# Kernel optimization log

Hardware: AMD Instinct MI355X
Metric: run time of the kernel (lower is better)

## Reference

```python
import jax, jax.numpy as jnp
import numpy as np

B, T, D = 64, 64, 256      # batch, decode steps, input_dim == wv_dim
TA = 128                   # encoder (attention) length
U = 256                    # units == att_dim
V = 50257                  # vocab_size


def hard_sigmoid(x):
    # keras hard_sigmoid
    return jnp.clip(0.2 * x + 0.5, 0.0, 1.0)


def setup_inputs() -> dict:
    key = jax.random.key(0)
    ks = jax.random.split(key, 8)
    n = lambda k, shape, sc: (jax.random.normal(k, shape, jnp.float32) * sc)
    return {
        "x": jax.random.normal(ks[0], (B, T, D), jnp.float32),
        "att": jax.random.normal(ks[1], (B, TA, U), jnp.float32),
        "kernel": n(ks[2], (D, 3 * U), 0.05),
        "recurrent_kernel": n(ks[3], (U, 3 * U), 0.05),
        "bias": jnp.zeros((3 * U,), jnp.float32),
        "after_att_kernel": n(ks[4], (U, 2 * U), 0.05),
        "after_att_bias": jnp.zeros((2 * U,), jnp.float32),
        "W_o1": n(ks[5], (U, V), 0.02),
        "embedding": n(ks[6], (V, D), 0.05),  # id2v table (non-trainable)
    }


def reference(x, att, kernel, recurrent_kernel, bias, after_att_kernel,
              after_att_bias, W_o1, embedding):
    u = recurrent_kernel.shape[0]
    # preprocess_input: time-distributed dense for all three gates at once
    xp = jnp.einsum('btd,dk->btk', x, kernel) + bias          # (B,T,3U)
    Kz, Kr, Kh = kernel[:, :u], kernel[:, u:2 * u], kernel[:, 2 * u:]
    Uz, Ur, Uh = (recurrent_kernel[:, :u], recurrent_kernel[:, u:2 * u],
                  recurrent_kernel[:, 2 * u:])
    Wa0, Wa1 = after_att_kernel[:, :u], after_att_kernel[:, u:2 * u]
    ba0, ba1 = after_att_bias[:u], after_att_bias[u:2 * u]

    h0 = jnp.zeros((x.shape[0], u), x.dtype)

    def step(h, xt):
        # attention over encoder outputs using previous hidden state
        e = jax.nn.softmax(jnp.einsum('btd,bd->bt', att, h))   # (B,TA)
        c = jnp.einsum('bt,btd->bd', e, att)                   # (B,U)
        # after-attention dense stack -> vocab distribution
        s = jnp.tanh(c @ Wa0 + ba0)
        s = jnp.tanh(s @ Wa1 + ba1)
        p = jax.nn.softmax(s @ W_o1)                           # (B,V)
        # embedding feedback (soft; hard_argmax=False)
        fb = p @ embedding                                     # (B,D)
        # GRU gates with feedback routed through the input kernel
        xz, xr, xh = xt[:, :u], xt[:, u:2 * u], xt[:, 2 * u:]
        z = hard_sigmoid(xz + fb @ Kz + h @ Uz)
        r = hard_sigmoid(xr + fb @ Kr + h @ Ur)
        hh = jnp.tanh(xh + fb @ Kh + (r * h) @ Uh)
        hn = z * h + (1.0 - z) * hh
        return hn, hn

    _, ys = jax.lax.scan(step, h0, jnp.swapaxes(xp, 0, 1))     # (T,B,U)
    return jnp.swapaxes(ys, 0, 1)                              # (B,T,U)
```

## Files before the change

### kernel.cpp

```cpp
#include <hip/hip_runtime.h>

#define BB 64
#define TT 64
#define DD 256
#define TAA 128
#define UU 256
#define VV 50257
#define NBLK 256
#define NV 208
#define NVK 224
#define W1ROWS 53248
#define EMBCOLS 53248
#define NT 512
#define OFF_W1   0
#define OFF_EMB  54912
#define OFF_P    114304
#define OFF_SA   129152
#define OFF_HL   146048
#define OFF_ZP   147072
#define SMEM_BYTES 147712

typedef __attribute__((ext_vector_type(4))) float floatx4;
typedef unsigned long long ull_t;

__device__ __forceinline__ float bf2f(unsigned short u) {
  union { unsigned int i; float f; } c; c.i = ((unsigned int)u) << 16; return c.f;
}
__device__ __forceinline__ float pklo(unsigned int u) { return __uint_as_float(u << 16); }
__device__ __forceinline__ float pkhi(unsigned int u) { return __uint_as_float(u & 0xffff0000u); }
__device__ __forceinline__ unsigned short f2bf(float f) {
  union { float f; unsigned int i; } c; c.f = f;
  return (unsigned short)((c.i + 0x7fffu + ((c.i >> 16) & 1u)) >> 16);
}
__device__ __forceinline__ float hsig(float x) {
  return fminf(1.0f, fmaxf(0.0f, 0.2f * x + 0.5f));
}
__device__ __forceinline__ unsigned int pk4_fp8(float a, float b, float c, float d) {
  unsigned int r = 0;
  r = __builtin_amdgcn_cvt_pk_fp8_f32(a, b, r, false);
  r = __builtin_amdgcn_cvt_pk_fp8_f32(c, d, r, true);
  return r;
}

__device__ __forceinline__ void st_f(float* p, float v) {
  __hip_atomic_store(p, v, __ATOMIC_RELAXED, __HIP_MEMORY_SCOPE_AGENT);
}
__device__ __forceinline__ float ld_f(const float* p) {
  return __hip_atomic_load(p, __ATOMIC_RELAXED, __HIP_MEMORY_SCOPE_AGENT);
}
__device__ __forceinline__ void st_u16(unsigned short* p, unsigned short v) {
  __hip_atomic_store(p, v, __ATOMIC_RELAXED, __HIP_MEMORY_SCOPE_AGENT);
}
__device__ __forceinline__ void st_u32(unsigned int* p, unsigned int v) {
  __hip_atomic_store(p, v, __ATOMIC_RELAXED, __HIP_MEMORY_SCOPE_AGENT);
}
__device__ __forceinline__ unsigned int ld_u32(const unsigned int* p) {
  return __hip_atomic_load(p, __ATOMIC_RELAXED, __HIP_MEMORY_SCOPE_AGENT);
}
__device__ __forceinline__ ull_t ld_u64(const ull_t* p) {
  return __hip_atomic_load(p, __ATOMIC_RELAXED, __HIP_MEMORY_SCOPE_AGENT);
}

__device__ __forceinline__ void gbar(ull_t* bar, int phase) {
  asm volatile("s_waitcnt vmcnt(0)" ::: "memory");
  __syncthreads();
  if (threadIdx.x == 0) {
    ull_t* myc = (ull_t*)((char*)bar + 128 * (1 + (blockIdx.x & 7)));
    ull_t t1 = __hip_atomic_fetch_add(myc, 1ull, __ATOMIC_RELAXED,
                                      __HIP_MEMORY_SCOPE_AGENT) + 1ull;
    if (t1 == (ull_t)(32 * phase)) {
      __hip_atomic_fetch_add(bar, 1ull, __ATOMIC_RELAXED, __HIP_MEMORY_SCOPE_AGENT);
    }
    while (__hip_atomic_load(bar, __ATOMIC_RELAXED, __HIP_MEMORY_SCOPE_AGENT) <
           (ull_t)(8 * phase))
      __builtin_amdgcn_s_sleep(4);
  }
  __syncthreads();
}


__global__ void k_f2bf(const float* __restrict__ in, unsigned short* __restrict__ out, int n) {
  int i = blockIdx.x * 256 + threadIdx.x;
  int stride = gridDim.x * 256;
  for (; i < n; i += stride) out[i] = f2bf(in[i]);
}

__global__ void k_pack(const float* __restrict__ kern, const float* __restrict__ rk,
                       unsigned int* __restrict__ kzr, unsigned int* __restrict__ uzr,
                       unsigned int* __restrict__ khu) {
  const int k = blockIdx.x;
  const int out = threadIdx.x;
  const float* kr0 = kern + (size_t)k * 768;
  const float* rr0 = rk + (size_t)k * 768;
  kzr[k * 256 + out] = (unsigned)f2bf(kr0[out]) | ((unsigned)f2bf(kr0[256 + out]) << 16);
  uzr[k * 256 + out] = (unsigned)f2bf(rr0[out]) | ((unsigned)f2bf(rr0[256 + out]) << 16);
  khu[k * 256 + out] = (unsigned)f2bf(kr0[512 + out]) | ((unsigned)f2bf(rr0[512 + out]) << 16);
}

__global__ void k_tw1(const float* __restrict__ w, unsigned int* __restrict__ o) {
  __shared__ float tile[32][33];
  const int bx = blockIdx.x, by = blockIdx.y;
  const int tx = threadIdx.x, ty = threadIdx.y;
#pragma unroll
  for (int i = 0; i < 4; ++i) {
    int k = by * 32 + ty + i * 8;
    int v = bx * 32 + tx;
    tile[ty + i * 8][tx] = (v < VV) ? w[(size_t)k * VV + v] : 0.0f;
  }
  __syncthreads();
  const int t = ty * 32 + tx;
  const int vl = t >> 3;
  const int cg = t & 7;
  unsigned int pk = pk4_fp8(tile[cg * 4 + 0][vl], tile[cg * 4 + 1][vl],
                            tile[cg * 4 + 2][vl], tile[cg * 4 + 3][vl]);
  o[(size_t)(bx * 32 + vl) * 64 + by * 8 + cg] = pk;
}

__global__ void k_temb(const float* __restrict__ e, unsigned int* __restrict__ o) {
  __shared__ float tile[32][33];
  const int bx = blockIdx.x, by = blockIdx.y;
  const int tx = threadIdx.x, ty = threadIdx.y;
#pragma unroll
  for (int i = 0; i < 4; ++i) {
    int v = bx * 32 + ty + i * 8;
    int d = by * 32 + tx;
    tile[ty + i * 8][tx] = (v < VV) ? e[(size_t)v * 256 + d] : 0.0f;
  }
  __syncthreads();
  const int t = ty * 32 + tx;
  const int dl = t >> 3;
  const int vg = t & 7;
  unsigned int pk = pk4_fp8(tile[vg * 4 + 0][dl], tile[vg * 4 + 1][dl],
                            tile[vg * 4 + 2][dl], tile[vg * 4 + 3][dl]);
  o[(size_t)(by * 32 + dl) * 13312 + bx * 8 + vg] = pk;
}

__global__ void k_xp(const float* __restrict__ x, const float* __restrict__ kern,
                     const float* __restrict__ bias, float* __restrict__ xp) {
  __shared__ float xs[256][20];
  const int r0 = blockIdx.x * 16;
  const int tid = threadIdx.x;
  for (int idx = tid; idx < 16 * 256; idx += 256) {
    int rr = idx >> 8;
    int k = idx & 255;
    xs[k][rr] = x[(size_t)(r0 + rr) * 256 + k];
  }
  __syncthreads();
  float acc[16][3];
#pragma unroll
  for (int rr = 0; rr < 16; ++rr) {
    acc[rr][0] = bias[tid];
    acc[rr][1] = bias[256 + tid];
    acc[rr][2] = bias[512 + tid];
  }
  for (int k = 0; k < 256; ++k) {
    float k0 = kern[k * 768 + tid];
    float k1 = kern[k * 768 + 256 + tid];
    float k2 = kern[k * 768 + 512 + tid];
#pragma unroll
    for (int rr = 0; rr < 16; ++rr) {
      float xv = xs[k][rr];
      acc[rr][0] = fmaf(xv, k0, acc[rr][0]);
      acc[rr][1] = fmaf(xv, k1, acc[rr][1]);
      acc[rr][2] = fmaf(xv, k2, acc[rr][2]);
    }
  }
  for (int rr = 0; rr < 16; ++rr) {
    xp[(size_t)(r0 + rr) * 768 + tid] = acc[rr][0];
    xp[(size_t)(r0 + rr) * 768 + 256 + tid] = acc[rr][1];
    xp[(size_t)(r0 + rr) * 768 + 512 + tid] = acc[rr][2];
  }
}


__global__ void __launch_bounds__(NT, 2) gru_main(
    const float* __restrict__ att,
    const float* __restrict__ aab,
    const unsigned int* __restrict__ kzr,
    const unsigned int* __restrict__ uzr,
    const unsigned int* __restrict__ khu,
    const unsigned short* __restrict__ aabf,
    const float* __restrict__ xp,
    const unsigned int* __restrict__ w1g,
    const unsigned int* __restrict__ embg,
    unsigned int* __restrict__ s8,
    unsigned short* __restrict__ pfb,
    float* __restrict__ psum,
    float* __restrict__ fbp4,
    ull_t* __restrict__ hflag,
    ull_t* __restrict__ bar,
    float* __restrict__ y)
{
  extern __shared__ char smem[];
  char* w1p  = smem + OFF_W1;
  char* embp = smem + OFF_EMB;
  char* Pp   = smem + OFF_P;
  char* sAp  = smem + OFF_SA;
  float* red4  = (float*)(smem + OFF_SA);
  float* fbL   = (float*)(smem + OFF_SA + 8192);
  float* rhL   = (float*)(smem + OFF_SA + 9216);
  float* cL    = (float*)(smem + OFF_SA + 10240);
  float* s1L   = (float*)(smem + OFF_SA + 11264);
  float* s2L   = (float*)(smem + OFF_SA + 12288);
  float* eL    = (float*)(smem + OFF_SA + 13312);
  float* zredL = (float*)(smem + OFF_SA + 13824);
  float* hL    = (float*)(smem + OFF_HL);
  float* zpartL= (float*)(smem + OFF_ZP);

  const int blk = blockIdx.x;
  const int tid = threadIdx.x;
  const int b = blk;
  const int vbase = blk * NV;

  const int w = tid >> 6;
  const int lane = tid & 63;
  const int w2 = w & 3;
  const int half = w >> 2;
  const int lq = lane >> 4;
  const int li = lane & 15;
  const int hb = blk & 63;
  const int hq = blk >> 6;

  {
    unsigned int* dst = (unsigned int*)w1p;
    for (int i = tid; i < NV * 64; i += NT) {
      int r = i >> 6, c = i & 63;
      dst[r * 66 + c] = w1g[(size_t)(vbase + r) * 64 + c];
    }
    unsigned int* ed = (unsigned int*)embp;
    for (int i = tid; i < 256 * 52; i += NT) {
      int r = i / 52, c = i - r * 52;
      ed[r * 58 + c] = embg[(size_t)r * 13312 + blk * 52 + c];
    }
    for (int i = tid; i < 256 * 6; i += NT) {
      int r = i / 6, c = i - r * 6;
      ed[r * 58 + 52 + c] = 0u;
    }
    unsigned int* Pd = (unsigned int*)Pp;
    for (int i = tid; i < 64 * 6; i += NT) {
      int r = i / 6, c = i - r * 6;
      Pd[r * 58 + 52 + c] = 0u;
    }
  }

  auto attention = [&]() {
    {
      const int r = tid >> 2, q = tid & 3;
      const float* ar = att + (size_t)(b * TAA + r) * DD + q * 64;
      const float* hp = hL + q * 64;
      float l0 = 0.f, l1 = 0.f;
#pragma unroll
      for (int dd = 0; dd < 64; dd += 8) {
        float4 a0 = *reinterpret_cast<const float4*>(ar + dd);
        float4 a1 = *reinterpret_cast<const float4*>(ar + dd + 4);
        l0 += a0.x * hp[dd] + a0.y * hp[dd + 1] + a0.z * hp[dd + 2] + a0.w * hp[dd + 3];
        l1 += a1.x * hp[dd + 4] + a1.y * hp[dd + 5] + a1.z * hp[dd + 6] + a1.w * hp[dd + 7];
      }
      float s = l0 + l1;
      s += __shfl_xor(s, 1);
      s += __shfl_xor(s, 2);
      if (q == 0) eL[r] = s;
    }
    __syncthreads();
    if (tid < 64) {
      float l0 = eL[tid], l1 = eL[tid + 64];
      float m = fmaxf(l0, l1);
#pragma unroll
      for (int off = 32; off > 0; off >>= 1) m = fmaxf(m, __shfl_xor(m, off));
      float e0 = __expf(l0 - m), e1 = __expf(l1 - m);
      float s = e0 + e1;
#pragma unroll
      for (int off = 32; off > 0; off >>= 1) s += __shfl_xor(s, off);
      float inv = 1.0f / s;
      eL[tid] = e0 * inv;
      eL[tid + 64] = e1 * inv;
    }
    __syncthreads();
    {
      const int d = tid & 255, g = tid >> 8;
      const float* ab = att + (size_t)b * TAA * DD + d;
      float c0 = 0.f, c1 = 0.f;
#pragma unroll 4
      for (int ta = g * 64; ta < g * 64 + 64; ta += 2) {
        c0 += eL[ta] * ab[(size_t)ta * DD];
        c1 += eL[ta + 1] * ab[(size_t)(ta + 1) * DD];
      }
      red4[tid] = c0 + c1;
    }
    __syncthreads();
    if (tid < 256) cL[tid] = red4[tid] + red4[tid + 256];
    __syncthreads();
    {
      const int out = tid & 255, g = tid >> 8;
      float a0 = g ? 0.f : aab[out], a1 = 0.f;
      for (int k = g * 128; k < g * 128 + 128; k += 2) {
        a0 += cL[k] * bf2f(aabf[k * 512 + out]);
        a1 += cL[k + 1] * bf2f(aabf[(k + 1) * 512 + out]);
      }
      red4[tid] = a0 + a1;
    }
    __syncthreads();
    if (tid < 256) s1L[tid] = tanhf(red4[tid] + red4[tid + 256]);
    __syncthreads();
    {
      const int out = tid & 255, g = tid >> 8;
      float a0 = g ? 0.f : aab[256 + out], a1 = 0.f;
      for (int k = g * 128; k < g * 128 + 128; k += 2) {
        a0 += s1L[k] * bf2f(aabf[k * 512 + 256 + out]);
        a1 += s1L[k + 1] * bf2f(aabf[(k + 1) * 512 + 256 + out]);
      }
      red4[tid] = a0 + a1;
    }
    __syncthreads();
    if (tid < 256) s2L[tid] = tanhf(red4[tid] + red4[tid + 256]);
    __syncthreads();
    if (tid < 64) {
      unsigned int pk = pk4_fp8(s2L[4 * tid], s2L[4 * tid + 1],
                                s2L[4 * tid + 2], s2L[4 * tid + 3]);
      st_u32(s8 + b * 64 + tid, pk);
    }
  };

  auto helper_reduce = [&]() {
    {
      const int gl = tid >> 6;
      const int dq = tid & 63;
      float a0 = 0, a1 = 0, a2 = 0, a3 = 0;
      const ull_t* base = (const ull_t*)pfb + (size_t)hb * (256 * 64) + dq;
      const int g0 = hq * 64 + gl;
#pragma unroll
      for (int i = 0; i < 8; ++i) {
        ull_t u = ld_u64(base + (size_t)(g0 + i * 8) * 64);
        a0 += __uint_as_float((unsigned)(u << 16));
        a1 += __uint_as_float((unsigned)u & 0xffff0000u);
        a2 += __uint_as_float(((unsigned)(u >> 16)) & 0xffff0000u);
        a3 += __uint_as_float(((unsigned)(u >> 32)) & 0xffff0000u);
      }
      *reinterpret_cast<float4*>(red4 + gl * 256 + dq * 4) =
          make_float4(a0, a1, a2, a3);
    }
    __syncthreads();
    if (tid < 256) {
      float s = 0.f;
#pragma unroll
      for (int j = 0; j < 8; ++j) s += red4[tid + j * 256];
      st_f(fbp4 + ((size_t)hb * 4 + hq) * 256 + tid, s);
    }
    asm volatile("s_waitcnt vmcnt(0)" ::: "memory");
    __syncthreads();
    if (tid == 0)
      __hip_atomic_fetch_add(hflag + (size_t)hb * 16, 1ull, __ATOMIC_RELAXED,
                             __HIP_MEMORY_SCOPE_AGENT);
  };

  auto ca_step = [&](int t) {
    if (tid < 256) zredL[tid] = ld_f(psum + b * 256 + tid);
    __syncthreads();
    if (tid < 64) {
      float z2 = zredL[tid] + zredL[tid + 64] + zredL[tid + 128] + zredL[tid + 192];
#pragma unroll
      for (int off = 32; off > 0; off >>= 1) z2 += __shfl_xor(z2, off);
      if (tid == 0) zredL[0] = z2;
    }
    if (tid == 0) {
      while (__hip_atomic_load(hflag + (size_t)b * 16, __ATOMIC_RELAXED,
                               __HIP_MEMORY_SCOPE_AGENT) < (ull_t)(4 * (t + 1)))
        __builtin_amdgcn_s_sleep(2);
    }
    __syncthreads();
    if (tid < 256) {
      float invZ = 1.0f / zredL[0];
      const float* fp = fbp4 + (size_t)b * 1024;
      fbL[tid] = (ld_f(fp + tid) + ld_f(fp + 256 + tid) +
                  ld_f(fp + 512 + tid) + ld_f(fp + 768 + tid)) * invZ;
    }
    __syncthreads();
    const float* xprow = xp + (size_t)(b * 64 + t) * 768;
    const int out = tid & 255, g = tid >> 8;
    float z0 = g ? 0.f : xprow[out], z1 = 0.f;
    float r0 = g ? 0.f : xprow[256 + out], r1 = 0.f;
    for (int k = g * 128; k < g * 128 + 128; k += 2) {
      float fb0 = fbL[k], h0 = hL[k], fb1 = fbL[k + 1], h1 = hL[k + 1];
      unsigned a0 = kzr[k * 256 + out];
      unsigned b0 = uzr[k * 256 + out];
      unsigned a1 = kzr[(k + 1) * 256 + out];
      unsigned b1 = uzr[(k + 1) * 256 + out];
      z0 += fb0 * pklo(a0) + h0 * pklo(b0);
      r0 += fb0 * pkhi(a0) + h0 * pkhi(b0);
      z1 += fb1 * pklo(a1) + h1 * pklo(b1);
      r1 += fb1 * pkhi(a1) + h1 * pkhi(b1);
    }
    red4[tid] = z0 + z1;
    red4[512 + tid] = r0 + r1;
    __syncthreads();
    float zf = 0.f;
    if (tid < 256) {
      zf = red4[tid] + red4[tid + 256];
      float rf = red4[512 + tid] + red4[768 + tid];
      rhL[tid] = hsig(rf) * hL[tid];
    }
    __syncthreads();
    {
      float hp0 = g ? 0.f : xprow[512 + out], hp1 = 0.f;
      for (int k = g * 128; k < g * 128 + 128; k += 2) {
        unsigned c0 = khu[k * 256 + out];
        unsigned c1 = khu[(k + 1) * 256 + out];
        hp0 += fbL[k] * pklo(c0) + rhL[k] * pkhi(c0);
        hp1 += fbL[k + 1] * pklo(c1) + rhL[k + 1] * pkhi(c1);
      }
      red4[1024 + tid] = hp0 + hp1;
    }
    __syncthreads();
    if (tid < 256) {
      float hh = tanhf(red4[1024 + tid] + red4[1280 + tid]);
      float z = hsig(zf);
      float hn = z * hL[tid] + (1.0f - z) * hh;
      y[(size_t)(b * 64 + t) * 256 + tid] = hn;
      hL[tid] = hn;
    }
    __syncthreads();
  };

  auto b_phase = [&]() {
    {
      unsigned int* sd = (unsigned int*)sAp;
      for (int i = tid; i < 4096; i += NT) {
        int r = i >> 6, c = i & 63;
        sd[r * 66 + c] = ld_u32(s8 + i);
      }
    }
    __syncthreads();
    long afr[8];
#pragma unroll
    for (int kk = 0; kk < 8; ++kk)
      afr[kk] = *reinterpret_cast<const long*>(sAp + (16 * w2 + li) * 264 + kk * 32 + lq * 8);
    float sacc[4] = {0.f, 0.f, 0.f, 0.f};
    const int vt0 = half ? 7 : 0;
    const int vt1 = half ? 13 : 7;
    for (int vt = vt0; vt < vt1; ++vt) {
      floatx4 lacc = (floatx4){0.f, 0.f, 0.f, 0.f};
#pragma unroll
      for (int kk = 0; kk < 8; ++kk) {
        long bfr = *reinterpret_cast<const long*>(w1p + (vt * 16 + li) * 264 + kk * 32 + lq * 8);
        lacc = __builtin_amdgcn_mfma_f32_16x16x32_fp8_fp8(afr[kk], bfr, lacc, 0, 0, 0);
      }
      const int v = vbase + vt * 16 + li;
      const bool ok = (v < VV);
#pragma unroll
      for (int q = 0; q < 4; ++q) {
        float p = ok ? __expf(lacc[q]) : 0.0f;
        sacc[q] += p;
        unsigned int pb = __builtin_amdgcn_cvt_pk_fp8_f32(p, 0.f, 0u, false);
        Pp[(16 * w2 + lq * 4 + q) * 232 + vt * 16 + li] = (char)(pb & 0xff);
      }
    }
#pragma unroll
    for (int q = 0; q < 4; ++q) {
      float s = sacc[q];
      s += __shfl_xor(s, 1);
      s += __shfl_xor(s, 2);
      s += __shfl_xor(s, 4);
      s += __shfl_xor(s, 8);
      if (li == 0) zpartL[(16 * w2 + lq * 4 + q) * 2 + half] = s;
    }
    __syncthreads();
    if (tid < 64) st_f(psum + tid * 256 + blk, zpartL[2 * tid] + zpartL[2 * tid + 1]);
    long pfr[7];
#pragma unroll
    for (int kk = 0; kk < 7; ++kk)
      pfr[kk] = *reinterpret_cast<const long*>(Pp + (16 * w2 + li) * 232 + kk * 32 + lq * 8);
    const int dt0 = half * 8;
#pragma unroll 4
    for (int dt = dt0; dt < dt0 + 8; ++dt) {
      floatx4 f = (floatx4){0.f, 0.f, 0.f, 0.f};
#pragma unroll
      for (int kk = 0; kk < 7; ++kk) {
        long efr = *reinterpret_cast<const long*>(embp + (dt * 16 + li) * 232 + kk * 32 + lq * 8);
        f = __builtin_amdgcn_mfma_f32_16x16x32_fp8_fp8(pfr[kk], efr, f, 0, 0, 0);
      }
#pragma unroll
      for (int q = 0; q < 4; ++q) {
        int row = 16 * w2 + lq * 4 + q;
        st_u16(pfb + ((size_t)(row * 256 + blk)) * 256 + dt * 16 + li, f2bf(f[q]));
      }
    }
  };

  __syncthreads();
  if (blk < BB) {
    if (tid < 256) hL[tid] = 0.0f;
    __syncthreads();
    attention();
  }
  gbar(bar, 1);
  for (int t = 0; t < TT; ++t) {
    b_phase();
    gbar(bar, 2 + 2 * t);
    helper_reduce();
    if (blk < BB) {
      ca_step(t);
      if (t + 1 < TT) attention();
    }
    gbar(bar, 3 + 2 * t);
  }
}


extern "C" void kernel_launch(void* const* d_in, const int* in_sizes, int n_in,
                              void* d_out, int out_size, void* d_ws, size_t ws_size,
                              hipStream_t stream) {
  const float* x    = (const float*)d_in[0];
  const float* att  = (const float*)d_in[1];
  const float* kern = (const float*)d_in[2];
  const float* rk   = (const float*)d_in[3];
  const float* bias = (const float*)d_in[4];
  const float* aak  = (const float*)d_in[5];
  const float* aab  = (const float*)d_in[6];
  const float* w1   = (const float*)d_in[7];
  const float* emb  = (const float*)d_in[8];
  float* y = (float*)d_out;

  char* ws = (char*)d_ws;
  size_t o = 0;
  auto alloc = [&](size_t bytes) {
    char* p = ws + o;
    o += (bytes + 255) & ~(size_t)255;
    return p;
  };
  ull_t* bar   = (ull_t*)alloc(2048);
  ull_t* hflag = (ull_t*)alloc(8192);
  unsigned int* w1g  = (unsigned int*)alloc((size_t)W1ROWS * 256);
  unsigned int* embg = (unsigned int*)alloc((size_t)256 * EMBCOLS);
  unsigned int* kzr  = (unsigned int*)alloc((size_t)256 * 256 * 4);
  unsigned int* uzr  = (unsigned int*)alloc((size_t)256 * 256 * 4);
  unsigned int* khu  = (unsigned int*)alloc((size_t)256 * 256 * 4);
  unsigned short* aabf = (unsigned short*)alloc((size_t)131072 * 2);
  float* xp  = (float*)alloc((size_t)4096 * 768 * 4);
  unsigned int* s8 = (unsigned int*)alloc((size_t)64 * 64 * 4);
  unsigned short* pfb = (unsigned short*)alloc((size_t)64 * 256 * 256 * 2);
  float* psum = (float*)alloc((size_t)64 * 256 * 4);
  float* fbp4 = (float*)alloc((size_t)64 * 4 * 256 * 4);
  (void)ws_size; (void)in_sizes; (void)n_in; (void)out_size;

  static bool attr_done = false;
  if (!attr_done) {
    hipFuncSetAttribute((const void*)gru_main,
                        hipFuncAttributeMaxDynamicSharedMemorySize, SMEM_BYTES);
    attr_done = true;
  }

  hipMemsetAsync(bar, 0, 2048 + 8192, stream);
  hipLaunchKernelGGL(k_pack, dim3(256), dim3(256), 0, stream, kern, rk, kzr, uzr, khu);
  hipLaunchKernelGGL(k_f2bf, dim3(512), dim3(256), 0, stream, aak, aabf, 131072);
  hipLaunchKernelGGL(k_tw1, dim3(1664, 8), dim3(32, 8), 0, stream, w1, w1g);
  hipLaunchKernelGGL(k_temb, dim3(1664, 8), dim3(32, 8), 0, stream, emb, embg);
  hipLaunchKernelGGL(k_xp, dim3(256), dim3(256), 0, stream, x, kern, bias, xp);
  hipLaunchKernelGGL(gru_main, dim3(NBLK), dim3(NT), SMEM_BYTES, stream,
                     att, aab, kzr, uzr, khu, aabf, xp, w1g, embg, s8, pfb, psum,
                     fbp4, hflag, bar, y);
}
```

Before: 2.882 ms.

## Let owner blocks reduce their own feedback quarter, pack dense weights in pairs

Owner blocks (blk < 64) now reduce the first quarter of their own feedback partials locally into shared memory instead of waiting on a helper block to write it to global memory. The flag wait therefore drops from four helper arrivals to three. The after-attention weights are packed as bf16 pairs so each load serves two k rows. The b_phase also reads the s8 A-fragments straight from global memory instead of staging them through shared memory behind an extra barrier. The trade-off is more work on the critical-path owner blocks and uncoalesced 64-bit global loads for the fragments.

```diff
diff --git a/kernel.cpp b/kernel.cpp
--- a/kernel.cpp
+++ b/kernel.cpp
@@ -79,12 +79,6 @@
 }
 
 
-__global__ void k_f2bf(const float* __restrict__ in, unsigned short* __restrict__ out, int n) {
-  int i = blockIdx.x * 256 + threadIdx.x;
-  int stride = gridDim.x * 256;
-  for (; i < n; i += stride) out[i] = f2bf(in[i]);
-}
-
 __global__ void k_pack(const float* __restrict__ kern, const float* __restrict__ rk,
                        unsigned int* __restrict__ kzr, unsigned int* __restrict__ uzr,
                        unsigned int* __restrict__ khu) {
@@ -97,6 +91,13 @@
   khu[k * 256 + out] = (unsigned)f2bf(kr0[512 + out]) | ((unsigned)f2bf(rr0[512 + out]) << 16);
 }
 
+__global__ void k_aap(const float* __restrict__ aak, unsigned int* __restrict__ aap2) {
+  const int idx = blockIdx.x * 256 + threadIdx.x;
+  const int k2 = idx >> 9, col = idx & 511;
+  aap2[idx] = (unsigned)f2bf(aak[(size_t)(2 * k2) * 512 + col]) |
+              ((unsigned)f2bf(aak[(size_t)(2 * k2 + 1) * 512 + col]) << 16);
+}
+
 __global__ void k_tw1(const float* __restrict__ w, unsigned int* __restrict__ o) {
   __shared__ float tile[32][33];
   const int bx = blockIdx.x, by = blockIdx.y;
@@ -179,7 +180,7 @@
     const unsigned int* __restrict__ kzr,
     const unsigned int* __restrict__ uzr,
     const unsigned int* __restrict__ khu,
-    const unsigned short* __restrict__ aabf,
+    const unsigned int* __restrict__ aap2,
     const float* __restrict__ xp,
     const unsigned int* __restrict__ w1g,
     const unsigned int* __restrict__ embg,
@@ -195,7 +196,6 @@
   char* w1p  = smem + OFF_W1;
   char* embp = smem + OFF_EMB;
   char* Pp   = smem + OFF_P;
-  char* sAp  = smem + OFF_SA;
   float* red4  = (float*)(smem + OFF_SA);
   float* fbL   = (float*)(smem + OFF_SA + 8192);
   float* rhL   = (float*)(smem + OFF_SA + 9216);
@@ -204,6 +204,7 @@
   float* s2L   = (float*)(smem + OFF_SA + 12288);
   float* eL    = (float*)(smem + OFF_SA + 13312);
   float* zredL = (float*)(smem + OFF_SA + 13824);
+  float* ownq  = (float*)(smem + OFF_SA + 14848);
   float* hL    = (float*)(smem + OFF_HL);
   float* zpartL= (float*)(smem + OFF_ZP);
 
@@ -293,9 +294,10 @@
     {
       const int out = tid & 255, g = tid >> 8;
       float a0 = g ? 0.f : aab[out], a1 = 0.f;
-      for (int k = g * 128; k < g * 128 + 128; k += 2) {
-        a0 += cL[k] * bf2f(aabf[k * 512 + out]);
-        a1 += cL[k + 1] * bf2f(aabf[(k + 1) * 512 + out]);
+      for (int k2 = g * 64; k2 < g * 64 + 64; ++k2) {
+        unsigned u = aap2[k2 * 512 + out];
+        a0 += cL[2 * k2] * pklo(u);
+        a1 += cL[2 * k2 + 1] * pkhi(u);
       }
       red4[tid] = a0 + a1;
     }
@@ -305,9 +307,10 @@
     {
       const int out = tid & 255, g = tid >> 8;
       float a0 = g ? 0.f : aab[256 + out], a1 = 0.f;
-      for (int k = g * 128; k < g * 128 + 128; k += 2) {
-        a0 += s1L[k] * bf2f(aabf[k * 512 + 256 + out]);
-        a1 += s1L[k + 1] * bf2f(aabf[(k + 1) * 512 + 256 + out]);
+      for (int k2 = g * 64; k2 < g * 64 + 64; ++k2) {
+        unsigned u = aap2[k2 * 512 + 256 + out];
+        a0 += s1L[2 * k2] * pklo(u);
+        a1 += s1L[2 * k2 + 1] * pkhi(u);
       }
       red4[tid] = a0 + a1;
     }
@@ -321,24 +324,26 @@
     }
   };
 
+  auto quarter_partials = [&](int thb, int thq) {
+    const int gl = tid >> 6;
+    const int dq = tid & 63;
+    float a0 = 0, a1 = 0, a2 = 0, a3 = 0;
+    const ull_t* base = (const ull_t*)pfb + (size_t)thb * (256 * 64) + dq;
+    const int g0 = thq * 64 + gl;
+#pragma unroll
+    for (int i = 0; i < 8; ++i) {
+      ull_t u = ld_u64(base + (size_t)(g0 + i * 8) * 64);
+      a0 += __uint_as_float((unsigned)(u << 16));
+      a1 += __uint_as_float((unsigned)u & 0xffff0000u);
+      a2 += __uint_as_float(((unsigned)(u >> 16)) & 0xffff0000u);
+      a3 += __uint_as_float(((unsigned)(u >> 32)) & 0xffff0000u);
+    }
+    *reinterpret_cast<float4*>(red4 + gl * 256 + dq * 4) =
+        make_float4(a0, a1, a2, a3);
+  };
+
   auto helper_reduce = [&]() {
-    {
-      const int gl = tid >> 6;
-      const int dq = tid & 63;
-      float a0 = 0, a1 = 0, a2 = 0, a3 = 0;
-      const ull_t* base = (const ull_t*)pfb + (size_t)hb * (256 * 64) + dq;
-      const int g0 = hq * 64 + gl;
-#pragma unroll
-      for (int i = 0; i < 8; ++i) {
-        ull_t u = ld_u64(base + (size_t)(g0 + i * 8) * 64);
-        a0 += __uint_as_float((unsigned)(u << 16));
-        a1 += __uint_as_float((unsigned)u & 0xffff0000u);
-        a2 += __uint_as_float(((unsigned)(u >> 16)) & 0xffff0000u);
-        a3 += __uint_as_float(((unsigned)(u >> 32)) & 0xffff0000u);
-      }
-      *reinterpret_cast<float4*>(red4 + gl * 256 + dq * 4) =
-          make_float4(a0, a1, a2, a3);
-    }
+    quarter_partials(hb, hq);
     __syncthreads();
     if (tid < 256) {
       float s = 0.f;
@@ -364,14 +369,14 @@
     }
     if (tid == 0) {
       while (__hip_atomic_load(hflag + (size_t)b * 16, __ATOMIC_RELAXED,
-                               __HIP_MEMORY_SCOPE_AGENT) < (ull_t)(4 * (t + 1)))
+                               __HIP_MEMORY_SCOPE_AGENT) < (ull_t)(3 * (t + 1)))
         __builtin_amdgcn_s_sleep(2);
     }
     __syncthreads();
     if (tid < 256) {
       float invZ = 1.0f / zredL[0];
       const float* fp = fbp4 + (size_t)b * 1024;
-      fbL[tid] = (ld_f(fp + tid) + ld_f(fp + 256 + tid) +
+      fbL[tid] = (ownq[tid] + ld_f(fp + 256 + tid) +
                   ld_f(fp + 512 + tid) + ld_f(fp + 768 + tid)) * invZ;
     }
     __syncthreads();
@@ -422,18 +427,10 @@
   };
 
   auto b_phase = [&]() {
-    {
-      unsigned int* sd = (unsigned int*)sAp;
-      for (int i = tid; i < 4096; i += NT) {
-        int r = i >> 6, c = i & 63;
-        sd[r * 66 + c] = ld_u32(s8 + i);
-      }
-    }
-    __syncthreads();
     long afr[8];
 #pragma unroll
     for (int kk = 0; kk < 8; ++kk)
-      afr[kk] = *reinterpret_cast<const long*>(sAp + (16 * w2 + li) * 264 + kk * 32 + lq * 8);
+      afr[kk] = (long)ld_u64((const ull_t*)s8 + (16 * w2 + li) * 32 + kk * 4 + lq);
     float sacc[4] = {0.f, 0.f, 0.f, 0.f};
     const int vt0 = half ? 7 : 0;
     const int vt1 = half ? 13 : 7;
@@ -496,10 +493,20 @@
   for (int t = 0; t < TT; ++t) {
     b_phase();
     gbar(bar, 2 + 2 * t);
-    helper_reduce();
     if (blk < BB) {
+      quarter_partials(b, 0);
+      __syncthreads();
+      if (tid < 256) {
+        float s = 0.f;
+#pragma unroll
+        for (int j = 0; j < 8; ++j) s += red4[tid + j * 256];
+        ownq[tid] = s;
+      }
+      __syncthreads();
       ca_step(t);
       if (t + 1 < TT) attention();
+    } else {
+      helper_reduce();
     }
     gbar(bar, 3 + 2 * t);
   }
@@ -534,7 +541,7 @@
   unsigned int* kzr  = (unsigned int*)alloc((size_t)256 * 256 * 4);
   unsigned int* uzr  = (unsigned int*)alloc((size_t)256 * 256 * 4);
   unsigned int* khu  = (unsigned int*)alloc((size_t)256 * 256 * 4);
-  unsigned short* aabf = (unsigned short*)alloc((size_t)131072 * 2);
+  unsigned int* aap2 = (unsigned int*)alloc((size_t)128 * 512 * 4);
   float* xp  = (float*)alloc((size_t)4096 * 768 * 4);
   unsigned int* s8 = (unsigned int*)alloc((size_t)64 * 64 * 4);
   unsigned short* pfb = (unsigned short*)alloc((size_t)64 * 256 * 256 * 2);
@@ -551,11 +558,11 @@
 
   hipMemsetAsync(bar, 0, 2048 + 8192, stream);
   hipLaunchKernelGGL(k_pack, dim3(256), dim3(256), 0, stream, kern, rk, kzr, uzr, khu);
-  hipLaunchKernelGGL(k_f2bf, dim3(512), dim3(256), 0, stream, aak, aabf, 131072);
+  hipLaunchKernelGGL(k_aap, dim3(256), dim3(256), 0, stream, aak, aap2);
   hipLaunchKernelGGL(k_tw1, dim3(1664, 8), dim3(32, 8), 0, stream, w1, w1g);
   hipLaunchKernelGGL(k_temb, dim3(1664, 8), dim3(32, 8), 0, stream, emb, embg);
   hipLaunchKernelGGL(k_xp, dim3(256), dim3(256), 0, stream, x, kern, bias, xp);
   hipLaunchKernelGGL(gru_main, dim3(NBLK), dim3(NT), SMEM_BYTES, stream,
-                     att, aab, kzr, uzr, khu, aabf, xp, w1g, embg, s8, pfb, psum,
+                     att, aab, kzr, uzr, khu, aap2, xp, w1g, embg, s8, pfb, psum,
                      fbp4, hflag, bar, y);
 }
```

Result: slower. 4.257 ms (+47.7%).
